# Kernel optimization log

Hardware: AMD Instinct MI355X
Metric: run time of the kernel (lower is better)

Reference implementation:

```python
import jax, jax.numpy as jnp
import numpy as np

N_SPANS = 2000
D_SPAN = 1220          # span representation dim (Test_Encoder docstring)
P = 65536              # number of (mention, antecedent) pairs
D_PHI = 60             # dist(20) + genre(20) + speaker(20)
IN_SIZE = 3 * D_SPAN + D_PHI  # 3720
HID = 150
BINS = np.array([1, 2, 3, 4, 5, 8, 16, 32, 64])


def setup_inputs() -> dict:
    key = jax.random.key(0)
    ks = jax.random.split(key, 16)
    inp = {
        "g_i": jax.random.normal(ks[0], (N_SPANS, D_SPAN), dtype=jnp.float32),
        "s_m": jax.random.normal(ks[1], (N_SPANS,), dtype=jnp.float32),
        "mention_ids": jax.random.randint(ks[2], (P,), 0, N_SPANS, dtype=jnp.int32),
        "antecedent_ids": jax.random.randint(ks[3], (P,), 0, N_SPANS, dtype=jnp.int32),
        "distances": jax.random.randint(ks[4], (P,), 1, 512, dtype=jnp.int32),
        "genres": jax.random.randint(ks[5], (P,), 0, 7, dtype=jnp.int32),
        "speakers": jax.random.randint(ks[6], (P,), 0, 3, dtype=jnp.int32),
        # embedding tables
        "dist_emb": jax.random.normal(ks[7], (len(BINS), 20), dtype=jnp.float32) * 0.1,
        "genre_emb": jax.random.normal(ks[8], (7, 20), dtype=jnp.float32) * 0.1,
        "speaker_emb": jax.random.normal(ks[9], (3, 20), dtype=jnp.float32) * 0.1,
        # FFNN params (fc1, fc2, fc3)
        "W1": jax.random.normal(ks[10], (IN_SIZE, HID), dtype=jnp.float32) / np.sqrt(IN_SIZE),
        "b1": jnp.zeros((HID,), dtype=jnp.float32),
        "W2": jax.random.normal(ks[11], (HID, HID), dtype=jnp.float32) / np.sqrt(HID),
        "b2": jnp.zeros((HID,), dtype=jnp.float32),
        "W3": jax.random.normal(ks[12], (HID, 1), dtype=jnp.float32) / np.sqrt(HID),
        "b3": jnp.zeros((1,), dtype=jnp.float32),
    }
    return inp


def _dist_to_bin(distances):
    # replicate Span_Distance_Embedding.dist_to_bin_id: bin id s.t. bins[id] <= d < bins[id+1],
    # last bin catches everything else (including d < 1, per the Python fallthrough).
    bins = jnp.asarray(BINS, dtype=jnp.int32)
    ids = jnp.searchsorted(bins, distances, side="right") - 1
    return jnp.clip(ids, 0, len(BINS) - 1)


def reference(g_i, s_m, mention_ids, antecedent_ids, distances, genres, speakers,
              dist_emb, genre_emb, speaker_emb, W1, b1, W2, b2, W3, b3):
    # phi_ij: concat of distance / genre / speaker embeddings   [P, 60]
    phi = jnp.concatenate(
        [dist_emb[_dist_to_bin(distances)], genre_emb[genres], speaker_emb[speakers]],
        axis=1)
    vec_i = g_i[mention_ids]        # [P, D]
    vec_j = g_i[antecedent_ids]     # [P, D]
    x = jnp.concatenate([vec_i, vec_j, vec_j * vec_j, phi], axis=1)  # [P, 3D+60]
    # FFNN (dropout inactive at eval)
    h = jax.nn.relu(x @ W1 + b1)
    h = jax.nn.relu(h @ W2 + b2)
    s_ij = (h @ W3 + b3)[:, 0]      # [P]
    coref_scores = s_m[mention_ids] + s_m[antecedent_ids] + s_ij
    return coref_scores
```

## Files before the change

### kernel.cpp

```cpp
#include <hip/hip_runtime.h>

typedef short bf16x8 __attribute__((ext_vector_type(8)));
typedef short bf16x4 __attribute__((ext_vector_type(4)));
typedef float f32x4  __attribute__((ext_vector_type(4)));

#define NSPAN 2000
#define DSPAN 1220
#define NPAIR 65536
#define HID   150
#define HP    160
#define TW    320
#define NKS   78
#define NKH   39
#define NMT   128
#define NNT   20
#define KC    6
#define H1S   168
#define NCMB  189

#define GA 1248
#define GB 390
#define GC 119
#define GD 13
#define GE 160

static __device__ __forceinline__ short f2bf(float x) {
  unsigned u = __builtin_bit_cast(unsigned, x);
  u = (u + 0x7FFFu + ((u >> 16) & 1u)) >> 16;
  return (short)u;
}

__global__ __launch_bounds__(256)
void prep_all(const float* __restrict__ g, const float* __restrict__ W1,
              const float* __restrict__ b1, const float* __restrict__ de,
              const float* __restrict__ ge, const float* __restrict__ se,
              const float* __restrict__ W2, short* __restrict__ A_fr,
              short* __restrict__ Wc_fr, float* __restrict__ combo,
              short* __restrict__ W2_fr, float* __restrict__ T) {
  int b = blockIdx.x;
  int t = threadIdx.x;
  if (b < GA) {
    int tid = b * 256 + t;
    int l  = tid & 63;
    int t2 = tid >> 6;
    int ks = t2 % NKH;
    int mt = t2 / NKH;
    int m  = mt * 16 + (l & 15);
    int k0 = ks * 32 + ((l >> 4) << 3);
    float x[8];
    if (m < NSPAN && k0 + 8 <= DSPAN) {
      float4 f0 = *(const float4*)&g[m * DSPAN + k0];
      float4 f1 = *(const float4*)&g[m * DSPAN + k0 + 4];
      x[0]=f0.x; x[1]=f0.y; x[2]=f0.z; x[3]=f0.w;
      x[4]=f1.x; x[5]=f1.y; x[6]=f1.z; x[7]=f1.w;
    } else {
#pragma unroll
      for (int i = 0; i < 8; ++i) {
        int k = k0 + i;
        x[i] = (m < NSPAN && k < DSPAN) ? g[m * DSPAN + k] : 0.f;
      }
    }
    short v1[8], v2[8];
#pragma unroll
    for (int i = 0; i < 8; ++i) { v1[i] = f2bf(x[i]); v2[i] = f2bf(x[i] * x[i]); }
    size_t o1 = ((size_t)(mt * NKS + ks) * 64 + l) * 8;
    *(bf16x8*)(A_fr + o1) = *(const bf16x8*)v1;
    *(bf16x8*)(A_fr + o1 + (size_t)NKH * 512) = *(const bf16x8*)v2;
  } else if (b < GA + GB) {
    int tid = (b - GA) * 256 + t;
    int l  = tid & 63;
    int t2 = tid >> 6;
    int ks = t2 % NKS;
    int nt = t2 / NKS;
    int n  = nt * 16 + (l & 15);
    int k0 = ks * 32 + ((l >> 4) << 3);
    short v[8];
#pragma unroll
    for (int i = 0; i < 8; ++i) {
      int k = k0 + i;
      float x = 0.f;
      if (n < HID) {
        if (k < DSPAN)                     x = W1[k * HID + n];
      } else if (n >= HP && n < HP + HID) {
        int j = n - HP;
        if (k < DSPAN)                     x = W1[(DSPAN + k) * HID + j];
        else if (k >= 1248 && k < 2468)    x = W1[(1192 + k) * HID + j];
      }
      v[i] = f2bf(x);
    }
    *(bf16x8*)(Wc_fr + (size_t)tid * 8) = *(const bf16x8*)v;
  } else if (b < GA + GB + GC) {
    int idx = (b - GA - GB) * 256 + t;
    if (idx < NCMB * HP) {
      int c = idx / HP;
      int j = idx - c * HP;
      float v = 0.f;
      if (j < HID) {
        int si = c % 3;
        int t2 = c / 3;
        int gi = t2 % 7;
        int bi = t2 / 7;
        v = b1[j];
        const float* dp = de + bi * 20;
        const float* gp = ge + gi * 20;
        const float* sp = se + si * 20;
#pragma unroll
        for (int e = 0; e < 20; ++e) {
          v += dp[e] * W1[(3660 + e) * HID + j];
          v += gp[e] * W1[(3680 + e) * HID + j];
          v += sp[e] * W1[(3700 + e) * HID + j];
        }
      }
      combo[idx] = v;
    }
  } else if (b < GA + GB + GC + GD) {
    int tid = (b - GA - GB - GC) * 256 + t;
    if (tid < 3200) {
      int l  = tid & 63;
      int t2 = tid >> 6;
      int ks = t2 % 5;
      int jt = t2 / 5;
      int n  = jt * 16 + (l & 15);
      int k0 = ks * 32 + ((l >> 4) << 3);
      short v[8];
#pragma unroll
      for (int i = 0; i < 8; ++i) {
        int k = k0 + i;
        float x = (k < HID && n < HID) ? W2[k * HID + n] : 0.f;
        v[i] = f2bf(x);
      }
      *(bf16x8*)(W2_fr + (size_t)tid * 8) = *(const bf16x8*)v;
    }
  } else {
    int idx = (b - GA - GB - GC - GD) * 256 + t;
    f32x4 z = {0.f, 0.f, 0.f, 0.f};
    if (idx < NSPAN * TW / 4) ((f32x4*)T)[idx] = z;
  }
}

__global__ __launch_bounds__(256)
void span_gemm(const short* __restrict__ A_fr, const short* __restrict__ Wc_fr,
               float* __restrict__ T) {
  int t = threadIdx.x, w = t >> 6, l = t & 63;
  int mt  = blockIdx.y * 4 + w;
  int ntb = blockIdx.x * 4;
  int ksb = blockIdx.z * 13;
  const short* pa = A_fr + ((size_t)(mt * NKS + ksb) * 64 + l) * 8;
  const short* pb = Wc_fr + ((size_t)(ntb * NKS + ksb) * 64 + l) * 8;
  f32x4 a0 = {0.f, 0.f, 0.f, 0.f}, a1 = a0, a2 = a0, a3 = a0;
#pragma unroll
  for (int ks = 0; ks < 13; ++ks) {
    bf16x8 a  = *(const bf16x8*)pa;
    bf16x8 b0 = *(const bf16x8*)pb;
    bf16x8 b1 = *(const bf16x8*)(pb + (size_t)NKS * 512);
    bf16x8 b2 = *(const bf16x8*)(pb + (size_t)2 * NKS * 512);
    bf16x8 b3 = *(const bf16x8*)(pb + (size_t)3 * NKS * 512);
    a0 = __builtin_amdgcn_mfma_f32_16x16x32_bf16(a, b0, a0, 0, 0, 0);
    a1 = __builtin_amdgcn_mfma_f32_16x16x32_bf16(a, b1, a1, 0, 0, 0);
    a2 = __builtin_amdgcn_mfma_f32_16x16x32_bf16(a, b2, a2, 0, 0, 0);
    a3 = __builtin_amdgcn_mfma_f32_16x16x32_bf16(a, b3, a3, 0, 0, 0);
    pa += 512; pb += 512;
  }
  int col = l & 15, row4 = (l >> 4) << 2;
  f32x4 acc[4] = {a0, a1, a2, a3};
#pragma unroll
  for (int r = 0; r < 4; ++r) {
    int m = mt * 16 + row4 + r;
    if (m < NSPAN) {
#pragma unroll
      for (int j = 0; j < 4; ++j)
        atomicAdd(&T[m * TW + (ntb + j) * 16 + col], acc[j][r]);
    }
  }
}

__global__ __launch_bounds__(256)
void pair_kernel(const float* __restrict__ T, const float* __restrict__ combo,
                 const short* __restrict__ W2_fr,
                 const float* __restrict__ b2, const float* __restrict__ W3,
                 const float* __restrict__ b3, const float* __restrict__ s_m,
                 const int* __restrict__ m_ids, const int* __restrict__ a_ids,
                 const int* __restrict__ dist, const int* __restrict__ genre,
                 const int* __restrict__ spk, float* __restrict__ out) {
  __shared__ short h1s[64 * H1S];
  __shared__ float w3s[HP], b2s[HP], sm2[64];
  __shared__ int mi[64], ai[64], co[64];

  int t = threadIdx.x;
  int base = blockIdx.x * 64;

  if (t < 64) {
    int p = base + t;
    int m = m_ids[p], a = a_ids[p];
    mi[t] = m; ai[t] = a;
    sm2[t] = s_m[m] + s_m[a];
    int d = dist[p];
    int bb = (d >= 2) + (d >= 3) + (d >= 4) + (d >= 5) + (d >= 8) +
             (d >= 16) + (d >= 32) + (d >= 64);
    co[t] = ((bb * 7 + genre[p]) * 3 + spk[p]) * HP;
  }
  if (t < HP) {
    w3s[t] = (t < HID) ? W3[t] : 0.f;
    b2s[t] = (t < HID) ? b2[t] : 0.f;
  }
  float b3v = b3[0];
  __syncthreads();

  for (int idx = t; idx < 64 * 40; idx += 256) {
    int p = idx / 40;
    int j = (idx - p * 40) * 4;
    const float4 vm = *(const float4*)&T[mi[p] * TW + j];
    const float4 va = *(const float4*)&T[ai[p] * TW + HP + j];
    const float4 fc = *(const float4*)&combo[co[p] + j];
    bf16x4 r;
    r[0] = f2bf(fmaxf(vm.x + va.x + fc.x, 0.f));
    r[1] = f2bf(fmaxf(vm.y + va.y + fc.y, 0.f));
    r[2] = f2bf(fmaxf(vm.z + va.z + fc.z, 0.f));
    r[3] = f2bf(fmaxf(vm.w + va.w + fc.w, 0.f));
    *(bf16x4*)&h1s[p * H1S + j] = r;
  }
  __syncthreads();

  int w = t >> 6, l = t & 63;
  const short* hrow = h1s + (w * 16 + (l & 15)) * H1S + ((l >> 4) << 3);
  bf16x8 af[5];
#pragma unroll
  for (int ks = 0; ks < 5; ++ks) af[ks] = *(const bf16x8*)(hrow + ks * 32);

  f32x4 acc[10];
#pragma unroll
  for (int jt = 0; jt < 10; ++jt) acc[jt] = {0.f, 0.f, 0.f, 0.f};

  const short* pw = W2_fr + l * 8;
#pragma unroll
  for (int jt = 0; jt < 10; ++jt) {
#pragma unroll
    for (int ks = 0; ks < 5; ++ks) {
      bf16x8 bfr = *(const bf16x8*)(pw + (size_t)(jt * 5 + ks) * 512);
      acc[jt] = __builtin_amdgcn_mfma_f32_16x16x32_bf16(af[ks], bfr, acc[jt], 0, 0, 0);
    }
  }

  float part[4] = {0.f, 0.f, 0.f, 0.f};
  int cl = l & 15;
#pragma unroll
  for (int jt = 0; jt < 10; ++jt) {
    int n = jt * 16 + cl;
    float w3v = w3s[n], b2v = b2s[n];
#pragma unroll
    for (int r = 0; r < 4; ++r) part[r] += fmaxf(acc[jt][r] + b2v, 0.f) * w3v;
  }
#pragma unroll
  for (int off = 8; off >= 1; off >>= 1) {
#pragma unroll
    for (int r = 0; r < 4; ++r) part[r] += __shfl_xor(part[r], off, 64);
  }
  if (cl == 0) {
    int rowb = (l >> 4) << 2;
#pragma unroll
    for (int r = 0; r < 4; ++r) {
      int p = w * 16 + rowb + r;
      out[base + p] = sm2[p] + part[r] + b3v;
    }
  }
}

extern "C" void kernel_launch(void* const* d_in, const int* in_sizes, int n_in,
                              void* d_out, int out_size, void* d_ws, size_t ws_size,
                              hipStream_t stream) {
  const float* g     = (const float*)d_in[0];
  const float* s_m   = (const float*)d_in[1];
  const int*   m_ids = (const int*)d_in[2];
  const int*   a_ids = (const int*)d_in[3];
  const int*   dist  = (const int*)d_in[4];
  const int*   genre = (const int*)d_in[5];
  const int*   spk   = (const int*)d_in[6];
  const float* de    = (const float*)d_in[7];
  const float* ge    = (const float*)d_in[8];
  const float* se    = (const float*)d_in[9];
  const float* W1    = (const float*)d_in[10];
  const float* b1    = (const float*)d_in[11];
  const float* W2    = (const float*)d_in[12];
  const float* b2    = (const float*)d_in[13];
  const float* W3    = (const float*)d_in[14];
  const float* b3    = (const float*)d_in[15];
  float* out = (float*)d_out;

  float* T     = (float*)d_ws;
  float* combo = T + NSPAN * TW;
  short* A_fr  = (short*)(combo + NCMB * HP);
  short* Wc_fr = A_fr + (size_t)NMT * NKS * 512;
  short* W2_fr = Wc_fr + (size_t)NNT * NKS * 512;

  prep_all<<<GA + GB + GC + GD + GE, 256, 0, stream>>>(
      g, W1, b1, de, ge, se, W2, A_fr, Wc_fr, combo, W2_fr, T);
  span_gemm<<<dim3(5, 32, KC), 256, 0, stream>>>(A_fr, Wc_fr, T);
  pair_kernel<<<NPAIR / 64, 256, 0, stream>>>(T, combo, W2_fr, b2, W3, b3, s_m,
                                              m_ids, a_ids, dist, genre, spk, out);
}
```

Measured before the change: 126.5 us.

## Replace split-K atomics with partial buffers plus bf16 reduce pass

The split-K span GEMM now writes per-slice partial results to separate buffers instead of using atomicAdd into a zeroed table. A new reduce kernel sums the six slices and stores the span table in bf16, and the combo table is also stored in bf16. The pair kernel then gathers half as many bytes per pair with 8-wide bf16 loads. This adds an extra kernel launch and about 15 MB of partial-buffer traffic, and it rounds the first-layer pre-activation terms to bf16 before they are summed.

```diff
diff --git a/kernel.cpp b/kernel.cpp
--- a/kernel.cpp
+++ b/kernel.cpp
@@ -17,17 +17,21 @@
 #define KC    6
 #define H1S   168
 #define NCMB  189
+#define TSZ   (NSPAN * TW)
 
 #define GA 1248
 #define GB 390
 #define GC 119
 #define GD 13
-#define GE 160
 
 static __device__ __forceinline__ short f2bf(float x) {
   unsigned u = __builtin_bit_cast(unsigned, x);
   u = (u + 0x7FFFu + ((u >> 16) & 1u)) >> 16;
   return (short)u;
+}
+static __device__ __forceinline__ float bf2f(short s) {
+  unsigned u = ((unsigned)(unsigned short)s) << 16;
+  return __builtin_bit_cast(float, u);
 }
 
 __global__ __launch_bounds__(256)
@@ -35,8 +39,8 @@
               const float* __restrict__ b1, const float* __restrict__ de,
               const float* __restrict__ ge, const float* __restrict__ se,
               const float* __restrict__ W2, short* __restrict__ A_fr,
-              short* __restrict__ Wc_fr, float* __restrict__ combo,
-              short* __restrict__ W2_fr, float* __restrict__ T) {
+              short* __restrict__ Wc_fr, short* __restrict__ combo,
+              short* __restrict__ W2_fr) {
   int b = blockIdx.x;
   int t = threadIdx.x;
   if (b < GA) {
@@ -111,9 +115,9 @@
           v += sp[e] * W1[(3700 + e) * HID + j];
         }
       }
-      combo[idx] = v;
-    }
-  } else if (b < GA + GB + GC + GD) {
+      combo[idx] = f2bf(v);
+    }
+  } else {
     int tid = (b - GA - GB - GC) * 256 + t;
     if (tid < 3200) {
       int l  = tid & 63;
@@ -131,20 +135,17 @@
       }
       *(bf16x8*)(W2_fr + (size_t)tid * 8) = *(const bf16x8*)v;
     }
-  } else {
-    int idx = (b - GA - GB - GC - GD) * 256 + t;
-    f32x4 z = {0.f, 0.f, 0.f, 0.f};
-    if (idx < NSPAN * TW / 4) ((f32x4*)T)[idx] = z;
   }
 }
 
 __global__ __launch_bounds__(256)
 void span_gemm(const short* __restrict__ A_fr, const short* __restrict__ Wc_fr,
-               float* __restrict__ T) {
+               float* __restrict__ Tpart) {
   int t = threadIdx.x, w = t >> 6, l = t & 63;
   int mt  = blockIdx.y * 4 + w;
   int ntb = blockIdx.x * 4;
   int ksb = blockIdx.z * 13;
+  float* Tp = Tpart + (size_t)blockIdx.z * TSZ;
   const short* pa = A_fr + ((size_t)(mt * NKS + ksb) * 64 + l) * 8;
   const short* pb = Wc_fr + ((size_t)(ntb * NKS + ksb) * 64 + l) * 8;
   f32x4 a0 = {0.f, 0.f, 0.f, 0.f}, a1 = a0, a2 = a0, a3 = a0;
@@ -169,13 +170,27 @@
     if (m < NSPAN) {
 #pragma unroll
       for (int j = 0; j < 4; ++j)
-        atomicAdd(&T[m * TW + (ntb + j) * 16 + col], acc[j][r]);
+        Tp[m * TW + (ntb + j) * 16 + col] = acc[j][r];
     }
   }
 }
 
 __global__ __launch_bounds__(256)
-void pair_kernel(const float* __restrict__ T, const float* __restrict__ combo,
+void reduce_T(const float* __restrict__ Tpart, short* __restrict__ Tb) {
+  int i = (blockIdx.x * 256 + threadIdx.x) * 4;
+  float4 s = *(const float4*)(Tpart + i);
+#pragma unroll
+  for (int z = 1; z < KC; ++z) {
+    float4 v = *(const float4*)(Tpart + (size_t)z * TSZ + i);
+    s.x += v.x; s.y += v.y; s.z += v.z; s.w += v.w;
+  }
+  bf16x4 r;
+  r[0] = f2bf(s.x); r[1] = f2bf(s.y); r[2] = f2bf(s.z); r[3] = f2bf(s.w);
+  *(bf16x4*)(Tb + i) = r;
+}
+
+__global__ __launch_bounds__(256)
+void pair_kernel(const short* __restrict__ Tb, const short* __restrict__ combo,
                  const short* __restrict__ W2_fr,
                  const float* __restrict__ b2, const float* __restrict__ W3,
                  const float* __restrict__ b3, const float* __restrict__ s_m,
@@ -206,18 +221,17 @@
   float b3v = b3[0];
   __syncthreads();
 
-  for (int idx = t; idx < 64 * 40; idx += 256) {
-    int p = idx / 40;
-    int j = (idx - p * 40) * 4;
-    const float4 vm = *(const float4*)&T[mi[p] * TW + j];
-    const float4 va = *(const float4*)&T[ai[p] * TW + HP + j];
-    const float4 fc = *(const float4*)&combo[co[p] + j];
-    bf16x4 r;
-    r[0] = f2bf(fmaxf(vm.x + va.x + fc.x, 0.f));
-    r[1] = f2bf(fmaxf(vm.y + va.y + fc.y, 0.f));
-    r[2] = f2bf(fmaxf(vm.z + va.z + fc.z, 0.f));
-    r[3] = f2bf(fmaxf(vm.w + va.w + fc.w, 0.f));
-    *(bf16x4*)&h1s[p * H1S + j] = r;
+  for (int idx = t; idx < 64 * 20; idx += 256) {
+    int p = idx / 20;
+    int j = (idx - p * 20) * 8;
+    bf16x8 va = *(const bf16x8*)&Tb[mi[p] * TW + j];
+    bf16x8 vb = *(const bf16x8*)&Tb[ai[p] * TW + HP + j];
+    bf16x8 vc = *(const bf16x8*)&combo[co[p] + j];
+    short r[8];
+#pragma unroll
+    for (int i = 0; i < 8; ++i)
+      r[i] = f2bf(fmaxf(bf2f(va[i]) + bf2f(vb[i]) + bf2f(vc[i]), 0.f));
+    *(bf16x8*)&h1s[p * H1S + j] = *(const bf16x8*)r;
   }
   __syncthreads();
 
@@ -259,8 +273,8 @@
     int rowb = (l >> 4) << 2;
 #pragma unroll
     for (int r = 0; r < 4; ++r) {
-      int p = w * 16 + rowb + r;
-      out[base + p] = sm2[p] + part[r] + b3v;
+      int pl = w * 16 + rowb + r;
+      out[base + pl] = sm2[pl] + part[r] + b3v;
     }
   }
 }
@@ -286,15 +300,17 @@
   const float* b3    = (const float*)d_in[15];
   float* out = (float*)d_out;
 
-  float* T     = (float*)d_ws;
-  float* combo = T + NSPAN * TW;
-  short* A_fr  = (short*)(combo + NCMB * HP);
+  float* Tpart = (float*)d_ws;
+  short* Tb    = (short*)(Tpart + (size_t)KC * TSZ);
+  short* combo = Tb + TSZ;
+  short* A_fr  = combo + NCMB * HP;
   short* Wc_fr = A_fr + (size_t)NMT * NKS * 512;
   short* W2_fr = Wc_fr + (size_t)NNT * NKS * 512;
 
-  prep_all<<<GA + GB + GC + GD + GE, 256, 0, stream>>>(
-      g, W1, b1, de, ge, se, W2, A_fr, Wc_fr, combo, W2_fr, T);
-  span_gemm<<<dim3(5, 32, KC), 256, 0, stream>>>(A_fr, Wc_fr, T);
-  pair_kernel<<<NPAIR / 64, 256, 0, stream>>>(T, combo, W2_fr, b2, W3, b3, s_m,
+  prep_all<<<GA + GB + GC + GD, 256, 0, stream>>>(
+      g, W1, b1, de, ge, se, W2, A_fr, Wc_fr, combo, W2_fr);
+  span_gemm<<<dim3(5, 32, KC), 256, 0, stream>>>(A_fr, Wc_fr, Tpart);
+  reduce_T<<<625, 256, 0, stream>>>(Tpart, Tb);
+  pair_kernel<<<NPAIR / 64, 256, 0, stream>>>(Tb, combo, W2_fr, b2, W3, b3, s_m,
                                               m_ids, a_ids, dist, genre, spk, out);
 }
```

After: 122.8 us. 1.03x faster.
